# Performance work log

Hardware: AMD Instinct MI355X
Metric: run time of the kernel (lower is better)

The kernel has to match this reference:

```python
import jax, jax.numpy as jnp
import numpy as np

EPS = 1e-7
MIN_NORM = 1e-15
PROJ_EPS = 1e-5
NEG_SLOPE = 0.2
HEADS = 4


def artanh(x):
    return jnp.arctanh(jnp.clip(x, -1.0 + EPS, 1.0 - EPS))


def _norm(x):
    return jnp.clip(jnp.linalg.norm(x, axis=-1, keepdims=True), MIN_NORM)


def proj(x):
    # project onto Poincare ball (c=1)
    n = _norm(x)
    maxn = 1.0 - PROJ_EPS
    return jnp.where(n > maxn, x / n * maxn, x)


def expmap0(u):
    n = _norm(u)
    return jnp.tanh(n) * u / n


def logmap0(x):
    n = _norm(x)
    return artanh(n) * x / n


def mobius_add(x, y):
    x2 = jnp.sum(x * x, axis=-1, keepdims=True)
    y2 = jnp.sum(y * y, axis=-1, keepdims=True)
    xy = jnp.sum(x * y, axis=-1, keepdims=True)
    num = (1.0 + 2.0 * xy + y2) * x + (1.0 - x2) * y
    den = 1.0 + 2.0 * xy + x2 * y2
    return num / jnp.clip(den, MIN_NORM)


def pdist(x, y):
    # Poincare distance, c=1 -> [...,] scalar
    ma = mobius_add(-x, y)
    return 2.0 * artanh(jnp.linalg.norm(ma, axis=-1))


def mobius_scalar_mul(r, x):
    n = _norm(x)
    return jnp.tanh(r * artanh(n)) * x / n


def mobius_matvec(W, x):
    # x: [N,din], W: [dout,din]
    mx = x @ W.T
    n_x = _norm(x)
    n_mx = _norm(mx)
    return jnp.tanh(n_mx / n_x * artanh(n_x)) * mx / n_mx


def segment_softmax(logits, seg, num_segments):
    m = jax.ops.segment_max(logits, seg, num_segments=num_segments)
    m = jnp.where(jnp.isfinite(m), m, 0.0)
    e = jnp.exp(logits - m[seg])
    s = jax.ops.segment_sum(e, seg, num_segments=num_segments)
    return e / (s[seg] + 1e-16)


def setup_inputs() -> dict:
    N, E, D = 50000, 500000, 128
    H = HEADS
    Dh = D // H
    ks = jax.random.split(jax.random.key(0), 12)
    # edges without self-loops (reference re-adds them, mirroring remove/add_self_loops)
    src = jax.random.randint(ks[0], (E,), 0, N)
    off = jax.random.randint(ks[1], (E,), 1, N)
    dst = (src + off) % N
    edge_index = jnp.stack([src, dst]).astype(jnp.int32)
    x_e = 0.1 * jax.random.normal(ks[2], (N, D), dtype=jnp.float32)
    x_h = proj(expmap0(0.05 * jax.random.normal(ks[3], (N, D), dtype=jnp.float32)))
    sc = 1.0 / np.sqrt(D)
    W_e = sc * jax.random.normal(ks[4], (D, D), dtype=jnp.float32)
    b_lin_e = jnp.zeros((D,), jnp.float32)
    att_e = 0.1 * jax.random.normal(ks[5], (1, H, 2 * Dh), dtype=jnp.float32)
    b_e = jnp.zeros((D,), jnp.float32)
    W_h = sc * jax.random.normal(ks[6], (D, D), dtype=jnp.float32)
    b_lin_h = jnp.zeros((D,), jnp.float32)
    att_h = 0.1 * jax.random.normal(ks[7], (1, H, 2 * Dh), dtype=jnp.float32)
    b_h = jnp.zeros((D,), jnp.float32)
    att_hf = 0.1 * jax.random.normal(ks[8], (1, 1), dtype=jnp.float32)
    att_ef = 0.1 * jax.random.normal(ks[9], (1, 1), dtype=jnp.float32)
    return {"x_e": x_e, "x_h": x_h, "edge_index": edge_index,
            "W_e": W_e, "b_lin_e": b_lin_e, "att_e": att_e, "b_e": b_e,
            "W_h": W_h, "b_lin_h": b_lin_h, "att_h": att_h, "b_h": b_h,
            "att_hf": att_hf, "att_ef": att_ef}


def reference(x_e, x_h, edge_index, W_e, b_lin_e, att_e, b_e,
              W_h, b_lin_h, att_h, b_h, att_hf, att_ef):
    N, D = x_e.shape
    H = HEADS
    Dh = att_e.shape[-1] // 2
    loop = jnp.arange(N, dtype=edge_index.dtype)
    src = jnp.concatenate([edge_index[0], loop])  # j (source)
    dst = jnp.concatenate([edge_index[1], loop])  # i (target, softmax segment)

    # ---- Euclidean GAT branch (GATConv) ----
    xe = (x_e @ W_e.T + b_lin_e).reshape(N, H, Dh)
    a_i = jnp.sum(xe * att_e[:, :, :Dh], axis=-1)  # [N,H] target part
    a_j = jnp.sum(xe * att_e[:, :, Dh:], axis=-1)  # [N,H] source part
    alpha = jax.nn.leaky_relu(a_i[dst] + a_j[src], NEG_SLOPE)  # [E',H]
    alpha = segment_softmax(alpha, dst, N)
    agg = jax.ops.segment_sum(xe[src] * alpha[:, :, None], dst, num_segments=N)
    e_out = jax.nn.relu(agg.reshape(N, H * Dh) + b_e)

    # ---- Hyperbolic GAT branch (HGATConv with HypLinear) ----
    mv = proj(mobius_matvec(W_h, x_h))
    hb = proj(expmap0(b_lin_h))  # proj_tan0 is identity on Poincare ball
    xh = proj(mobius_add(mv, hb))  # [N,D] hyperbolic points (original_x)
    lx = logmap0(xh).reshape(N, H, Dh)
    hi = jnp.sum(lx * att_h[:, :, :Dh], axis=-1)
    hj = jnp.sum(lx * att_h[:, :, Dh:], axis=-1)
    alpha_h = hi[dst] + hj[src]  # [E',H]
    d = pdist(xh[dst], xh[src])  # [E'] hyperbolic edge distances
    d = segment_softmax(d, dst, N)[:, None]
    alpha_h = jax.nn.leaky_relu(alpha_h * d, NEG_SLOPE)
    alpha_h = segment_softmax(alpha_h, dst, N)
    agg_h = jax.ops.segment_sum(lx[src] * alpha_h[:, :, None], dst, num_segments=N)
    out_t = jax.nn.relu(agg_h.reshape(N, H * Dh) + b_h)  # tangent at origin
    h_out = proj(expmap0(out_t))

    # ---- HFusion: fuse Euclidean into hyperbolic ----
    ye = proj(expmap0(e_out))
    dist_f = (pdist(h_out, ye) * att_hf[0, 0])[:, None]  # [N,1]
    xe2 = proj(mobius_scalar_mul(dist_f, ye))
    h_fused = proj(mobius_add(h_out, xe2))

    # ---- EFusion: fuse hyperbolic into Euclidean ----
    lh = logmap0(h_out)
    de = (jnp.sum((lh - e_out) ** 2, axis=-1) * att_ef[0, 0])[:, None]
    e_fused = e_out + de * lh

    return jnp.stack([h_fused, e_fused])  # [2,N,D]
```

## Files before the change

### kernel.cpp

```cpp
#include <hip/hip_runtime.h>
#include <hip/hip_fp16.h>
#include <math.h>

typedef _Float16 h2 __attribute__((ext_vector_type(2)));
typedef _Float16 h8 __attribute__((ext_vector_type(8)));
typedef float f32x4 __attribute__((ext_vector_type(4)));

#define MAXN_BALL (1.0f - 1e-5f)
#define ART_CLIP  (1.0f - 1e-7f)
#define MAXD 48

__device__ __forceinline__ float f_rcp(float x)  { return __builtin_amdgcn_rcpf(x); }
__device__ __forceinline__ float f_exp(float x)  { return __expf(x); }
__device__ __forceinline__ float f_log(float x)  { return __logf(x); }
__device__ __forceinline__ float f_tanh(float x) {
    float ax = fabsf(x);
    float e = __expf(2.f * ax);
    float t = 1.f - 2.f * f_rcp(e + 1.f);
    return copysignf(t, x);
}
__device__ __forceinline__ float f_atanh(float x) {
    x = fminf(x, ART_CLIP);
    return 0.5f * f_log((1.f + x) * f_rcp(1.f - x));
}
__device__ __forceinline__ float leaky(float x) { return x > 0.0f ? x : 0.2f * x; }

union F4H8 { float4 f; h2 h[4]; };
union F2H4 { float2 f; h2 h[2]; };
union H8U  { h8 v; h2 h[4]; };

__device__ __forceinline__ h2 pk16(float x, float y) {
    union { decltype(__builtin_amdgcn_cvt_pkrtz(0.f, 0.f)) a; h2 b; } u;
    u.a = __builtin_amdgcn_cvt_pkrtz(x, y);
    return u.b;
}

__global__ __launch_bounds__(256) void k_prep(const float* __restrict__ X0,
                                              const float* __restrict__ X1,
                                              const float* __restrict__ W0,
                                              const float* __restrict__ W1,
                                              const float* __restrict__ bias0,
                                              h2* __restrict__ Y0,
                                              h2* __restrict__ Y1,
                                              int* __restrict__ counts,
                                              int N) {
    int t = threadIdx.x;
    if (blockIdx.y == 0) {
        int zi = blockIdx.x * 256 + t;
        if (zi < N) counts[zi] = 0;
    }
    int wv = t >> 6, l = t & 63;
    int rt = blockIdx.x * 4 + wv;
    if (rt * 16 >= N) return;
    int mat = blockIdx.y;
    const float* X = mat ? X1 : X0;
    const float* W = mat ? W1 : W0;
    h2* Y = mat ? Y1 : Y0;

    int lane16 = l & 15, quad = l >> 4;
    int r = rt * 16 + lane16;
    int rr = (r < N) ? r : (N - 1);
    const float* Xrow = &X[(size_t)rr * 128 + quad * 8];

    H8U bfr[4];
#pragma unroll
    for (int ks = 0; ks < 4; ++ks) {
        float4 xa = *(const float4*)(Xrow + ks * 32);
        float4 xb = *(const float4*)(Xrow + ks * 32 + 4);
        bfr[ks].h[0] = pk16(xa.x, xa.y); bfr[ks].h[1] = pk16(xa.z, xa.w);
        bfr[ks].h[2] = pk16(xb.x, xb.y); bfr[ks].h[3] = pk16(xb.z, xb.w);
    }

#pragma unroll
    for (int ct = 0; ct < 8; ++ct) {
        int o = ct * 16 + lane16;
        const float* Wrow = &W[(size_t)o * 128 + quad * 8];
        f32x4 acc = {0.f, 0.f, 0.f, 0.f};
#pragma unroll
        for (int ks = 0; ks < 4; ++ks) {
            float4 wa = *(const float4*)(Wrow + ks * 32);
            float4 wb = *(const float4*)(Wrow + ks * 32 + 4);
            H8U a;
            a.h[0] = pk16(wa.x, wa.y); a.h[1] = pk16(wa.z, wa.w);
            a.h[2] = pk16(wb.x, wb.y); a.h[3] = pk16(wb.z, wb.w);
            acc = __builtin_amdgcn_mfma_f32_16x16x32_f16(a.v, bfr[ks].v, acc, 0, 0, 0);
        }
        int obase = ct * 16 + quad * 4;
        float b0 = 0.f, b1 = 0.f, b2 = 0.f, b3 = 0.f;
        if (mat == 0) {
            b0 = bias0[obase]; b1 = bias0[obase + 1];
            b2 = bias0[obase + 2]; b3 = bias0[obase + 3];
        }
        if (r < N) {
            F2H4 u;
            u.h[0] = pk16(acc[0] + b0, acc[1] + b1);
            u.h[1] = pk16(acc[2] + b2, acc[3] + b3);
            *(float2*)&Y[(size_t)r * 64 + (obase >> 1)] = u.f;
        }
    }
}

__global__ __launch_bounds__(256) void k_node1_scatter(
        const h2* __restrict__ xe16, const float* __restrict__ x_h,
        const h2* __restrict__ mx16, h2* __restrict__ xh16,
        float* __restrict__ aux_j, float* __restrict__ aux_i,
        const float* __restrict__ att_e, const float* __restrict__ att_h,
        const float* __restrict__ b_lin_h,
        const int* __restrict__ ei, int* __restrict__ counts,
        int* __restrict__ srcs,
        int N, int E, int nblocks) {
    int t = threadIdx.x;
    int bx = blockIdx.x;
    if (bx >= nblocks) {
        int idx = (bx - nblocks) * 256 + t;
        if (idx < E + N) {
            int s, d;
            if (idx < E) { s = ei[idx]; d = ei[E + idx]; } else { s = d = idx - E; }
            int p = atomicAdd(&counts[d], 1);
            if (p < MAXD) srcs[d * MAXD + p] = s;
        }
        return;
    }
    int sl = t & 31, ni = t >> 5;
    int i = bx * 8 + ni;
    if (i >= N) return;
    int ht = sl >> 3, d0 = (sl & 7) * 4;

    F2H4 uxe; uxe.f = *(const float2*)&xe16[(size_t)i * 64 + 2 * sl];
    float4 xe4 = make_float4((float)uxe.h[0].x, (float)uxe.h[0].y,
                             (float)uxe.h[1].x, (float)uxe.h[1].y);
    float4 aeT = *(const float4*)&att_e[ht * 64 + d0];
    float4 aeS = *(const float4*)&att_e[ht * 64 + 32 + d0];
    float pi = xe4.x * aeT.x + xe4.y * aeT.y + xe4.z * aeT.z + xe4.w * aeT.w;
    float pj = xe4.x * aeS.x + xe4.y * aeS.y + xe4.z * aeS.z + xe4.w * aeS.w;
#pragma unroll
    for (int m = 1; m <= 4; m <<= 1) { pi += __shfl_xor(pi, m, 64); pj += __shfl_xor(pj, m, 64); }

    F2H4 umx; umx.f = *(const float2*)&mx16[(size_t)i * 64 + 2 * sl];
    float4 mx4 = make_float4((float)umx.h[0].x, (float)umx.h[0].y,
                             (float)umx.h[1].x, (float)umx.h[1].y);
    float4 xv4 = *(const float4*)&x_h[(size_t)i * 128 + 4 * sl];
    float4 bv4 = *(const float4*)&b_lin_h[4 * sl];
    float nx2  = xv4.x * xv4.x + xv4.y * xv4.y + xv4.z * xv4.z + xv4.w * xv4.w;
    float nmx2 = mx4.x * mx4.x + mx4.y * mx4.y + mx4.z * mx4.z + mx4.w * mx4.w;
    float nb2  = bv4.x * bv4.x + bv4.y * bv4.y + bv4.z * bv4.z + bv4.w * bv4.w;
    float dmb  = mx4.x * bv4.x + mx4.y * bv4.y + mx4.z * bv4.z + mx4.w * bv4.w;
#pragma unroll
    for (int m = 16; m >= 1; m >>= 1) {
        nx2 += __shfl_xor(nx2, m, 64); nmx2 += __shfl_xor(nmx2, m, 64);
        nb2 += __shfl_xor(nb2, m, 64); dmb  += __shfl_xor(dmb, m, 64);
    }

    float nxr = sqrtf(nx2),  nxc = fmaxf(nxr, 1e-15f);
    float nmxr = sqrtf(nmx2), nmxc = fmaxf(nmxr, 1e-15f);
    float tt = f_tanh(nmxc * f_rcp(nxc) * f_atanh(nxc));
    float c_m = tt * f_rcp(nmxc);
    float nmv = tt * (nmxr * f_rcp(nmxc));
    if (nmv > MAXN_BALL) { c_m *= MAXN_BALL / nmv; nmv = MAXN_BALL; }

    float nbr = sqrtf(nb2), nbc = fmaxf(nbr, 1e-15f);
    float tb = f_tanh(nbc);
    float c_b = tb * f_rcp(nbc);
    float nhb = tb * (nbr * f_rcp(nbc));
    if (nhb > MAXN_BALL) { c_b *= MAXN_BALL / nhb; nhb = MAXN_BALL; }

    float xy = c_m * c_b * dmb;
    float x2 = nmv * nmv, y2 = nhb * nhb;
    float den = fmaxf(1.f + 2.f * xy + x2 * y2, 1e-15f);
    float rden = f_rcp(den);
    float al = (1.f + 2.f * xy + y2) * c_m * rden;
    float be = (1.f - x2) * c_b * rden;
    float nr2 = al * al * nmx2 + 2.f * al * be * dmb + be * be * nb2;
    float nrr = sqrtf(nr2);
    if (nrr > MAXN_BALL) { float sc = MAXN_BALL / nrr; al *= sc; be *= sc; }
    float4 resv;
    resv.x = al * mx4.x + be * bv4.x; resv.y = al * mx4.y + be * bv4.y;
    resv.z = al * mx4.z + be * bv4.z; resv.w = al * mx4.w + be * bv4.w;
    F2H4 st;
    st.h[0] = pk16(resv.x, resv.y);
    st.h[1] = pk16(resv.z, resv.w);
    *(float2*)&xh16[(size_t)i * 64 + 2 * sl] = st.f;
    float4 rv = make_float4((float)st.h[0].x, (float)st.h[0].y,
                            (float)st.h[1].x, (float)st.h[1].y);

    float nr2r = rv.x * rv.x + rv.y * rv.y + rv.z * rv.z + rv.w * rv.w;
#pragma unroll
    for (int m = 16; m >= 1; m >>= 1) nr2r += __shfl_xor(nr2r, m, 64);
    float nrrr = sqrtf(nr2r);
    float nnc = fmaxf(nrrr, 1e-15f);
    float lam = f_atanh(nnc) * f_rcp(nnc);
    if (sl == 0) { aux_j[(size_t)i * 16 + 8] = lam; aux_j[(size_t)i * 16 + 9] = nr2r; }

    float4 lxv = make_float4(lam * rv.x, lam * rv.y, lam * rv.z, lam * rv.w);
    float4 ahT = *(const float4*)&att_h[ht * 64 + d0];
    float4 ahS = *(const float4*)&att_h[ht * 64 + 32 + d0];
    float qi = lxv.x * ahT.x + lxv.y * ahT.y + lxv.z * ahT.z + lxv.w * ahT.w;
    float qj = lxv.x * ahS.x + lxv.y * ahS.y + lxv.z * ahS.z + lxv.w * ahS.w;
#pragma unroll
    for (int m = 1; m <= 4; m <<= 1) { qi += __shfl_xor(qi, m, 64); qj += __shfl_xor(qj, m, 64); }
    if ((sl & 7) == 0) {
        aux_j[(size_t)i * 16 + ht] = qj;
        aux_j[(size_t)i * 16 + 4 + ht] = pj;
        aux_i[(size_t)i * 8 + ht] = qi;
        aux_i[(size_t)i * 8 + 4 + ht] = pi;
    }
}

__global__ __launch_bounds__(256) void k_node_final(
    const h2* __restrict__ xh16, const float* __restrict__ aux_j,
    const float* __restrict__ aux_i, const h2* __restrict__ xe16,
    const int* __restrict__ counts, const int* __restrict__ srcs,
    const float* __restrict__ b_e, const float* __restrict__ b_h,
    const float* __restrict__ att_hf, const float* __restrict__ att_ef,
    float* __restrict__ out, int N) {
    __shared__ int   s_src_all[8][MAXD];
    __shared__ float s_d_all[8][MAXD];
    __shared__ float s_ah_all[8][MAXD * 4];
    __shared__ float s_ae_all[8][MAXD * 4];

    int t = threadIdx.x;
    int sl = t & 31, ni = t >> 5;
    int i = blockIdx.x * 8 + ni;
    if (i >= N) return;
    int*   s_src = s_src_all[ni];
    float* s_d   = s_d_all[ni];
    float* s_ah  = s_ah_all[ni];
    float* s_ae  = s_ae_all[ni];

    int deg = counts[i];
    if (deg > MAXD) deg = MAXD;
    if (sl < deg)      s_src[sl]      = srcs[i * MAXD + sl];
    if (sl + 32 < deg) s_src[sl + 32] = srcs[i * MAXD + sl + 32];

    float x2i = aux_j[(size_t)i * 16 + 9];
    {
        int g = sl & 7, sub = sl >> 3;
        const h2* xi = &xh16[(size_t)i * 64 + g * 8];
        F4H8 us0, us1;
        us0.f = *(const float4*)xi;
        us1.f = *(const float4*)(xi + 4);
        for (int p = 0; p * 4 < deg; ++p) {
            int e = p * 4 + sub;
            bool act = e < deg;
            float dot = 0.f;
            int j = 0;
            if (act) {
                j = s_src[e];
                const h2* rp = &xh16[(size_t)j * 64 + g * 8];
                F4H8 ua, ub;
                ua.f = *(const float4*)rp;
                ub.f = *(const float4*)(rp + 4);
#pragma unroll
                for (int k = 0; k < 4; ++k) dot = __builtin_amdgcn_fdot2(ua.h[k], us0.h[k], dot, false);
#pragma unroll
                for (int k = 0; k < 4; ++k) dot = __builtin_amdgcn_fdot2(ub.h[k], us1.h[k], dot, false);
            }
            dot += __shfl_xor(dot, 1, 64);
            dot += __shfl_xor(dot, 2, 64);
            dot += __shfl_xor(dot, 4, 64);
            if (act && g == 0) {
                float y2 = aux_j[(size_t)j * 16 + 9];
                float xy = dot;
                float A = 1.f - 2.f * xy + y2;
                float B = 1.f - x2i;
                float den = fmaxf(1.f - 2.f * xy + x2i * y2, 1e-15f);
                float num2 = fmaxf(A * A * x2i - 2.f * A * B * xy + B * B * y2, 0.f);
                float nma = fminf(sqrtf(num2) * f_rcp(den), ART_CLIP);
                s_d[e] = f_log((1.f + nma) * f_rcp(1.f - nma));
            }
        }
    }

    float eA = (sl < deg)      ? f_exp(s_d[sl])      : 0.f;
    float eB = (sl + 32 < deg) ? f_exp(s_d[sl + 32]) : 0.f;
    float ssum = eA + eB;
#pragma unroll
    for (int m = 16; m >= 1; m >>= 1) ssum += __shfl_xor(ssum, m, 64);
    float dinv = f_rcp(ssum + 1e-16f);

    float4 hi4 = *(const float4*)&aux_i[(size_t)i * 8];
    float4 ai4 = *(const float4*)&aux_i[(size_t)i * 8 + 4];
    float4 vh_s[2], ve_s[2];
    float lam_s[2] = {0.f, 0.f};
    float4 sh = make_float4(0.f, 0.f, 0.f, 0.f), se = sh;
#pragma unroll
    for (int s = 0; s < 2; ++s) {
        int e = sl + 32 * s;
        if (e < deg) {
            int j = s_src[e];
            float ds = (s ? eB : eA) * dinv;
            float4 hj4 = *(const float4*)&aux_j[(size_t)j * 16];
            float4 aj4 = *(const float4*)&aux_j[(size_t)j * 16 + 4];
            lam_s[s] = aux_j[(size_t)j * 16 + 8];
            float4 vh, ve;
            vh.x = f_exp(leaky((hi4.x + hj4.x) * ds));
            vh.y = f_exp(leaky((hi4.y + hj4.y) * ds));
            vh.z = f_exp(leaky((hi4.z + hj4.z) * ds));
            vh.w = f_exp(leaky((hi4.w + hj4.w) * ds));
            ve.x = f_exp(leaky(ai4.x + aj4.x));
            ve.y = f_exp(leaky(ai4.y + aj4.y));
            ve.z = f_exp(leaky(ai4.z + aj4.z));
            ve.w = f_exp(leaky(ai4.w + aj4.w));
            vh_s[s] = vh; ve_s[s] = ve;
            sh.x += vh.x; sh.y += vh.y; sh.z += vh.z; sh.w += vh.w;
            se.x += ve.x; se.y += ve.y; se.z += ve.z; se.w += ve.w;
        }
    }
#pragma unroll
    for (int m = 16; m >= 1; m >>= 1) {
        sh.x += __shfl_xor(sh.x, m, 64); sh.y += __shfl_xor(sh.y, m, 64);
        sh.z += __shfl_xor(sh.z, m, 64); sh.w += __shfl_xor(sh.w, m, 64);
        se.x += __shfl_xor(se.x, m, 64); se.y += __shfl_xor(se.y, m, 64);
        se.z += __shfl_xor(se.z, m, 64); se.w += __shfl_xor(se.w, m, 64);
    }
    float4 rh = make_float4(f_rcp(sh.x + 1e-16f), f_rcp(sh.y + 1e-16f),
                            f_rcp(sh.z + 1e-16f), f_rcp(sh.w + 1e-16f));
    float4 re = make_float4(f_rcp(se.x + 1e-16f), f_rcp(se.y + 1e-16f),
                            f_rcp(se.z + 1e-16f), f_rcp(se.w + 1e-16f));
#pragma unroll
    for (int s = 0; s < 2; ++s) {
        int e = sl + 32 * s;
        if (e < deg) {
            float lamj = lam_s[s];
            float4 vh = vh_s[s], ve = ve_s[s];
            vh.x *= rh.x * lamj; vh.y *= rh.y * lamj; vh.z *= rh.z * lamj; vh.w *= rh.w * lamj;
            ve.x *= re.x; ve.y *= re.y; ve.z *= re.z; ve.w *= re.w;
            *(float4*)&s_ah[e * 4] = vh;
            *(float4*)&s_ae[e * 4] = ve;
        }
    }

    int hq = sl >> 3;
    float4 aE = make_float4(0.f, 0.f, 0.f, 0.f), aH = aE;
    int e = 0;
    for (; e + 1 < deg; e += 2) {
        int j0 = s_src[e], j1 = s_src[e + 1];
        F2H4 ux0, uh0, ux1, uh1;
        ux0.f = *(const float2*)&xe16[(size_t)j0 * 64 + 2 * sl];
        uh0.f = *(const float2*)&xh16[(size_t)j0 * 64 + 2 * sl];
        ux1.f = *(const float2*)&xe16[(size_t)j1 * 64 + 2 * sl];
        uh1.f = *(const float2*)&xh16[(size_t)j1 * 64 + 2 * sl];
        float we0 = s_ae[e * 4 + hq], wh0 = s_ah[e * 4 + hq];
        float we1 = s_ae[(e + 1) * 4 + hq], wh1 = s_ah[(e + 1) * 4 + hq];
        aE.x += we0 * (float)ux0.h[0].x + we1 * (float)ux1.h[0].x;
        aE.y += we0 * (float)ux0.h[0].y + we1 * (float)ux1.h[0].y;
        aE.z += we0 * (float)ux0.h[1].x + we1 * (float)ux1.h[1].x;
        aE.w += we0 * (float)ux0.h[1].y + we1 * (float)ux1.h[1].y;
        aH.x += wh0 * (float)uh0.h[0].x + wh1 * (float)uh1.h[0].x;
        aH.y += wh0 * (float)uh0.h[0].y + wh1 * (float)uh1.h[0].y;
        aH.z += wh0 * (float)uh0.h[1].x + wh1 * (float)uh1.h[1].x;
        aH.w += wh0 * (float)uh0.h[1].y + wh1 * (float)uh1.h[1].y;
    }
    if (e < deg) {
        int j = s_src[e];
        F2H4 ux, uh;
        ux.f = *(const float2*)&xe16[(size_t)j * 64 + 2 * sl];
        uh.f = *(const float2*)&xh16[(size_t)j * 64 + 2 * sl];
        float we = s_ae[e * 4 + hq], wh = s_ah[e * 4 + hq];
        aE.x += we * (float)ux.h[0].x; aE.y += we * (float)ux.h[0].y;
        aE.z += we * (float)ux.h[1].x; aE.w += we * (float)ux.h[1].y;
        aH.x += wh * (float)uh.h[0].x; aH.y += wh * (float)uh.h[0].y;
        aH.z += wh * (float)uh.h[1].x; aH.w += wh * (float)uh.h[1].y;
    }

    float4 be4 = *(const float4*)&b_e[4 * sl];
    float4 bh4 = *(const float4*)&b_h[4 * sl];
    float4 eo, ot;
    eo.x = fmaxf(aE.x + be4.x, 0.f); eo.y = fmaxf(aE.y + be4.y, 0.f);
    eo.z = fmaxf(aE.z + be4.z, 0.f); eo.w = fmaxf(aE.w + be4.w, 0.f);
    ot.x = fmaxf(aH.x + bh4.x, 0.f); ot.y = fmaxf(aH.y + bh4.y, 0.f);
    ot.z = fmaxf(aH.z + bh4.z, 0.f); ot.w = fmaxf(aH.w + bh4.w, 0.f);
    float n2  = ot.x * ot.x + ot.y * ot.y + ot.z * ot.z + ot.w * ot.w;
    float ne2 = eo.x * eo.x + eo.y * eo.y + eo.z * eo.z + eo.w * eo.w;
    float dot3 = ot.x * eo.x + ot.y * eo.y + ot.z * eo.z + ot.w * eo.w;
#pragma unroll
    for (int m = 16; m >= 1; m >>= 1) {
        n2 += __shfl_xor(n2, m, 64); ne2 += __shfl_xor(ne2, m, 64); dot3 += __shfl_xor(dot3, m, 64);
    }

    float n_raw = sqrtf(n2), n_c = fmaxf(n_raw, 1e-15f);
    float th = f_tanh(n_c);
    float c_h = th * f_rcp(n_c);
    float nh = th * (n_raw * f_rcp(n_c));
    if (nh > MAXN_BALL) { c_h *= MAXN_BALL / nh; nh = MAXN_BALL; }

    float nE_raw = sqrtf(ne2), nE_c = fmaxf(nE_raw, 1e-15f);
    float tE = f_tanh(nE_c);
    float c_e = tE * f_rcp(nE_c);
    float ny = tE * (nE_raw * f_rcp(nE_c));
    if (ny > MAXN_BALL) { c_e *= MAXN_BALL / ny; ny = MAXN_BALL; }

    float xyv = c_h * c_e * dot3;
    float x2f = nh * nh, y2f = ny * ny;
    float A = 1.f - 2.f * xyv + y2f, B = 1.f - x2f;
    float den = fmaxf(1.f - 2.f * xyv + x2f * y2f, 1e-15f);
    float num2 = fmaxf(A * A * x2f - 2.f * A * B * xyv + B * B * y2f, 0.f);
    float nma = fminf(sqrtf(num2) * f_rcp(den), ART_CLIP);
    float distf = f_log((1.f + nma) * f_rcp(1.f - nma)) * att_hf[0];
    float nyc = fmaxf(ny, 1e-15f);
    float s1 = f_tanh(distf * f_atanh(nyc)) * f_rcp(nyc);
    float nxe2 = fabsf(s1) * ny;
    if (nxe2 > MAXN_BALL) { s1 *= MAXN_BALL / nxe2; nxe2 = MAXN_BALL; }
    float xy2 = s1 * xyv;
    float y22 = nxe2 * nxe2;
    float rden2 = f_rcp(fmaxf(1.f + 2.f * xy2 + x2f * y22, 1e-15f));
    float alpha = (1.f + 2.f * xy2 + y22) * rden2 * c_h;
    float beta  = (1.f - x2f) * s1 * rden2 * c_e;
    float nf2 = alpha * alpha * n2 + 2.f * alpha * beta * dot3 + beta * beta * ne2;
    float nf = sqrtf(nf2);
    if (nf > MAXN_BALL) { float sc = MAXN_BALL / nf; alpha *= sc; beta *= sc; }

    float nhc = fmaxf(nh, 1e-15f);
    float gam = f_atanh(nhc) * f_rcp(nhc) * c_h;
    float de2 = gam * gam * n2 - 2.f * gam * dot3 + ne2;
    float dg = de2 * att_ef[0] * gam;

    float4 o1;
    o1.x = alpha * ot.x + beta * eo.x; o1.y = alpha * ot.y + beta * eo.y;
    o1.z = alpha * ot.z + beta * eo.z; o1.w = alpha * ot.w + beta * eo.w;
    *(float4*)&out[(size_t)i * 128 + 4 * sl] = o1;
    float4 o2;
    o2.x = eo.x + dg * ot.x; o2.y = eo.y + dg * ot.y;
    o2.z = eo.z + dg * ot.z; o2.w = eo.w + dg * ot.w;
    *(float4*)&out[(size_t)N * 128 + (size_t)i * 128 + 4 * sl] = o2;
}

extern "C" void kernel_launch(void* const* d_in, const int* in_sizes, int n_in,
                              void* d_out, int out_size, void* d_ws, size_t ws_size,
                              hipStream_t stream) {
    const float* x_e      = (const float*)d_in[0];
    const float* x_h      = (const float*)d_in[1];
    const int*   ei       = (const int*)d_in[2];
    const float* W_e      = (const float*)d_in[3];
    const float* b_lin_e  = (const float*)d_in[4];
    const float* att_e    = (const float*)d_in[5];
    const float* b_e      = (const float*)d_in[6];
    const float* W_h      = (const float*)d_in[7];
    const float* b_lin_h  = (const float*)d_in[8];
    const float* att_h    = (const float*)d_in[9];
    const float* b_h      = (const float*)d_in[10];
    const float* att_hf   = (const float*)d_in[11];
    const float* att_ef   = (const float*)d_in[12];

    int N = in_sizes[0] / 128;
    int E = in_sizes[2] / 2;
    int EN = E + N;

    char* ws = (char*)d_ws;
    size_t off = 0;
    auto alloc = [&](size_t bytes) -> void* {
        void* p = ws + off;
        off = (off + bytes + 255) & ~(size_t)255;
        return p;
    };
    h2*    xe16  = (h2*)alloc((size_t)N * 128 * 2);
    h2*    mx16  = (h2*)alloc((size_t)N * 128 * 2);
    h2*    xh16  = (h2*)alloc((size_t)N * 128 * 2);
    float* aux_j = (float*)alloc((size_t)N * 16 * 4);
    float* aux_i = (float*)alloc((size_t)N * 8 * 4);
    int*   counts= (int*)alloc((size_t)N * 4);
    int*   srcs  = (int*)alloc((size_t)N * MAXD * 4);

    int rtiles = (N + 15) / 16;
    int rblocks = (rtiles + 3) / 4;
    dim3 pgrid(rblocks, 2);
    k_prep<<<pgrid, 256, 0, stream>>>(x_e, x_h, W_e, W_h, b_lin_e,
                                      xe16, mx16, counts, N);

    int nblocks = (N + 7) / 8;
    int eblocks = (EN + 255) / 256;
    k_node1_scatter<<<nblocks + eblocks, 256, 0, stream>>>(
        xe16, x_h, mx16, xh16, aux_j, aux_i,
        att_e, att_h, b_lin_h, ei, counts, srcs, N, E, nblocks);

    int fblocks = (N + 7) / 8;
    k_node_final<<<fblocks, 256, 0, stream>>>(xh16, aux_j, aux_i, xe16,
                                              counts, srcs, b_e, b_h, att_hf, att_ef,
                                              (float*)d_out, N);
}
```

Baseline: 290.4 us.

## Interleave Euclidean and hyperbolic fp16 features into one buffer; unroll distance loop

```diff
diff --git a/kernel.cpp b/kernel.cpp
--- a/kernel.cpp
+++ b/kernel.cpp
@@ -40,8 +40,7 @@
                                               const float* __restrict__ W0,
                                               const float* __restrict__ W1,
                                               const float* __restrict__ bias0,
-                                              h2* __restrict__ Y0,
-                                              h2* __restrict__ Y1,
+                                              float* __restrict__ xd,
                                               int* __restrict__ counts,
                                               int N) {
     int t = threadIdx.x;
@@ -55,7 +54,6 @@
     int mat = blockIdx.y;
     const float* X = mat ? X1 : X0;
     const float* W = mat ? W1 : W0;
-    h2* Y = mat ? Y1 : Y0;
 
     int lane16 = l & 15, quad = l >> 4;
     int r = rt * 16 + lane16;
@@ -95,14 +93,14 @@
             F2H4 u;
             u.h[0] = pk16(acc[0] + b0, acc[1] + b1);
             u.h[1] = pk16(acc[2] + b2, acc[3] + b3);
-            *(float2*)&Y[(size_t)r * 64 + (obase >> 1)] = u.f;
+            *(float2*)&xd[(size_t)r * 128 + obase + (mat ? 2 : 0)] = u.f;
         }
     }
 }
 
 __global__ __launch_bounds__(256) void k_node1_scatter(
-        const h2* __restrict__ xe16, const float* __restrict__ x_h,
-        const h2* __restrict__ mx16, h2* __restrict__ xh16,
+        float* __restrict__ xd, const float* __restrict__ x_h,
+        h2* __restrict__ xh16,
         float* __restrict__ aux_j, float* __restrict__ aux_i,
         const float* __restrict__ att_e, const float* __restrict__ att_h,
         const float* __restrict__ b_lin_h,
@@ -126,7 +124,7 @@
     if (i >= N) return;
     int ht = sl >> 3, d0 = (sl & 7) * 4;
 
-    F2H4 uxe; uxe.f = *(const float2*)&xe16[(size_t)i * 64 + 2 * sl];
+    F2H4 uxe; uxe.f = *(const float2*)&xd[(size_t)i * 128 + 4 * sl];
     float4 xe4 = make_float4((float)uxe.h[0].x, (float)uxe.h[0].y,
                              (float)uxe.h[1].x, (float)uxe.h[1].y);
     float4 aeT = *(const float4*)&att_e[ht * 64 + d0];
@@ -136,7 +134,7 @@
 #pragma unroll
     for (int m = 1; m <= 4; m <<= 1) { pi += __shfl_xor(pi, m, 64); pj += __shfl_xor(pj, m, 64); }
 
-    F2H4 umx; umx.f = *(const float2*)&mx16[(size_t)i * 64 + 2 * sl];
+    F2H4 umx; umx.f = *(const float2*)&xd[(size_t)i * 128 + 4 * sl + 2];
     float4 mx4 = make_float4((float)umx.h[0].x, (float)umx.h[0].y,
                              (float)umx.h[1].x, (float)umx.h[1].y);
     float4 xv4 = *(const float4*)&x_h[(size_t)i * 128 + 4 * sl];
@@ -180,6 +178,7 @@
     st.h[0] = pk16(resv.x, resv.y);
     st.h[1] = pk16(resv.z, resv.w);
     *(float2*)&xh16[(size_t)i * 64 + 2 * sl] = st.f;
+    *(float2*)&xd[(size_t)i * 128 + 4 * sl + 2] = st.f;
     float4 rv = make_float4((float)st.h[0].x, (float)st.h[0].y,
                             (float)st.h[1].x, (float)st.h[1].y);
 
@@ -207,8 +206,8 @@
 }
 
 __global__ __launch_bounds__(256) void k_node_final(
-    const h2* __restrict__ xh16, const float* __restrict__ aux_j,
-    const float* __restrict__ aux_i, const h2* __restrict__ xe16,
+    const h2* __restrict__ xh16, const float* __restrict__ xd,
+    const float* __restrict__ aux_j, const float* __restrict__ aux_i,
     const int* __restrict__ counts, const int* __restrict__ srcs,
     const float* __restrict__ b_e, const float* __restrict__ b_h,
     const float* __restrict__ att_hf, const float* __restrict__ att_ef,
@@ -239,34 +238,61 @@
         F4H8 us0, us1;
         us0.f = *(const float4*)xi;
         us1.f = *(const float4*)(xi + 4);
-        for (int p = 0; p * 4 < deg; ++p) {
-            int e = p * 4 + sub;
-            bool act = e < deg;
-            float dot = 0.f;
-            int j = 0;
-            if (act) {
-                j = s_src[e];
-                const h2* rp = &xh16[(size_t)j * 64 + g * 8];
-                F4H8 ua, ub;
-                ua.f = *(const float4*)rp;
-                ub.f = *(const float4*)(rp + 4);
-#pragma unroll
-                for (int k = 0; k < 4; ++k) dot = __builtin_amdgcn_fdot2(ua.h[k], us0.h[k], dot, false);
-#pragma unroll
-                for (int k = 0; k < 4; ++k) dot = __builtin_amdgcn_fdot2(ub.h[k], us1.h[k], dot, false);
+        for (int p = 0; p * 8 < deg; ++p) {
+            int e0 = p * 8 + sub;
+            int e1 = e0 + 4;
+            bool a0 = e0 < deg, a1 = e1 < deg;
+            float dot0 = 0.f, dot1 = 0.f;
+            int j0 = 0, j1 = 0;
+            F4H8 ua0, ub0, ua1, ub1;
+            if (a0) {
+                j0 = s_src[e0];
+                const h2* rp = &xh16[(size_t)j0 * 64 + g * 8];
+                ua0.f = *(const float4*)rp;
+                ub0.f = *(const float4*)(rp + 4);
             }
-            dot += __shfl_xor(dot, 1, 64);
-            dot += __shfl_xor(dot, 2, 64);
-            dot += __shfl_xor(dot, 4, 64);
-            if (act && g == 0) {
-                float y2 = aux_j[(size_t)j * 16 + 9];
-                float xy = dot;
-                float A = 1.f - 2.f * xy + y2;
-                float B = 1.f - x2i;
-                float den = fmaxf(1.f - 2.f * xy + x2i * y2, 1e-15f);
-                float num2 = fmaxf(A * A * x2i - 2.f * A * B * xy + B * B * y2, 0.f);
-                float nma = fminf(sqrtf(num2) * f_rcp(den), ART_CLIP);
-                s_d[e] = f_log((1.f + nma) * f_rcp(1.f - nma));
+            if (a1) {
+                j1 = s_src[e1];
+                const h2* rp = &xh16[(size_t)j1 * 64 + g * 8];
+                ua1.f = *(const float4*)rp;
+                ub1.f = *(const float4*)(rp + 4);
+            }
+            if (a0) {
+#pragma unroll
+                for (int k = 0; k < 4; ++k) dot0 = __builtin_amdgcn_fdot2(ua0.h[k], us0.h[k], dot0, false);
+#pragma unroll
+                for (int k = 0; k < 4; ++k) dot0 = __builtin_amdgcn_fdot2(ub0.h[k], us1.h[k], dot0, false);
+            }
+            if (a1) {
+#pragma unroll
+                for (int k = 0; k < 4; ++k) dot1 = __builtin_amdgcn_fdot2(ua1.h[k], us0.h[k], dot1, false);
+#pragma unroll
+                for (int k = 0; k < 4; ++k) dot1 = __builtin_amdgcn_fdot2(ub1.h[k], us1.h[k], dot1, false);
+            }
+            dot0 += __shfl_xor(dot0, 1, 64); dot1 += __shfl_xor(dot1, 1, 64);
+            dot0 += __shfl_xor(dot0, 2, 64); dot1 += __shfl_xor(dot1, 2, 64);
+            dot0 += __shfl_xor(dot0, 4, 64); dot1 += __shfl_xor(dot1, 4, 64);
+            if (g == 0) {
+                if (a0) {
+                    float y2 = aux_j[(size_t)j0 * 16 + 9];
+                    float xy = dot0;
+                    float A = 1.f - 2.f * xy + y2;
+                    float B = 1.f - x2i;
+                    float den = fmaxf(1.f - 2.f * xy + x2i * y2, 1e-15f);
+                    float num2 = fmaxf(A * A * x2i - 2.f * A * B * xy + B * B * y2, 0.f);
+                    float nma = fminf(sqrtf(num2) * f_rcp(den), ART_CLIP);
+                    s_d[e0] = f_log((1.f + nma) * f_rcp(1.f - nma));
+                }
+                if (a1) {
+                    float y2 = aux_j[(size_t)j1 * 16 + 9];
+                    float xy = dot1;
+                    float A = 1.f - 2.f * xy + y2;
+                    float B = 1.f - x2i;
+                    float den = fmaxf(1.f - 2.f * xy + x2i * y2, 1e-15f);
+                    float num2 = fmaxf(A * A * x2i - 2.f * A * B * xy + B * B * y2, 0.f);
+                    float nma = fminf(sqrtf(num2) * f_rcp(den), ART_CLIP);
+                    s_d[e1] = f_log((1.f + nma) * f_rcp(1.f - nma));
+                }
             }
         }
     }
@@ -335,32 +361,29 @@
     int e = 0;
     for (; e + 1 < deg; e += 2) {
         int j0 = s_src[e], j1 = s_src[e + 1];
-        F2H4 ux0, uh0, ux1, uh1;
-        ux0.f = *(const float2*)&xe16[(size_t)j0 * 64 + 2 * sl];
-        uh0.f = *(const float2*)&xh16[(size_t)j0 * 64 + 2 * sl];
-        ux1.f = *(const float2*)&xe16[(size_t)j1 * 64 + 2 * sl];
-        uh1.f = *(const float2*)&xh16[(size_t)j1 * 64 + 2 * sl];
+        F4H8 u0, u1;
+        u0.f = *(const float4*)&xd[(size_t)j0 * 128 + 4 * sl];
+        u1.f = *(const float4*)&xd[(size_t)j1 * 128 + 4 * sl];
         float we0 = s_ae[e * 4 + hq], wh0 = s_ah[e * 4 + hq];
         float we1 = s_ae[(e + 1) * 4 + hq], wh1 = s_ah[(e + 1) * 4 + hq];
-        aE.x += we0 * (float)ux0.h[0].x + we1 * (float)ux1.h[0].x;
-        aE.y += we0 * (float)ux0.h[0].y + we1 * (float)ux1.h[0].y;
-        aE.z += we0 * (float)ux0.h[1].x + we1 * (float)ux1.h[1].x;
-        aE.w += we0 * (float)ux0.h[1].y + we1 * (float)ux1.h[1].y;
-        aH.x += wh0 * (float)uh0.h[0].x + wh1 * (float)uh1.h[0].x;
-        aH.y += wh0 * (float)uh0.h[0].y + wh1 * (float)uh1.h[0].y;
-        aH.z += wh0 * (float)uh0.h[1].x + wh1 * (float)uh1.h[1].x;
-        aH.w += wh0 * (float)uh0.h[1].y + wh1 * (float)uh1.h[1].y;
+        aE.x += we0 * (float)u0.h[0].x + we1 * (float)u1.h[0].x;
+        aE.y += we0 * (float)u0.h[0].y + we1 * (float)u1.h[0].y;
+        aE.z += we0 * (float)u0.h[1].x + we1 * (float)u1.h[1].x;
+        aE.w += we0 * (float)u0.h[1].y + we1 * (float)u1.h[1].y;
+        aH.x += wh0 * (float)u0.h[2].x + wh1 * (float)u1.h[2].x;
+        aH.y += wh0 * (float)u0.h[2].y + wh1 * (float)u1.h[2].y;
+        aH.z += wh0 * (float)u0.h[3].x + wh1 * (float)u1.h[3].x;
+        aH.w += wh0 * (float)u0.h[3].y + wh1 * (float)u1.h[3].y;
     }
     if (e < deg) {
         int j = s_src[e];
-        F2H4 ux, uh;
-        ux.f = *(const float2*)&xe16[(size_t)j * 64 + 2 * sl];
-        uh.f = *(const float2*)&xh16[(size_t)j * 64 + 2 * sl];
+        F4H8 u0;
+        u0.f = *(const float4*)&xd[(size_t)j * 128 + 4 * sl];
         float we = s_ae[e * 4 + hq], wh = s_ah[e * 4 + hq];
-        aE.x += we * (float)ux.h[0].x; aE.y += we * (float)ux.h[0].y;
-        aE.z += we * (float)ux.h[1].x; aE.w += we * (float)ux.h[1].y;
-        aH.x += wh * (float)uh.h[0].x; aH.y += wh * (float)uh.h[0].y;
-        aH.z += wh * (float)uh.h[1].x; aH.w += wh * (float)uh.h[1].y;
+        aE.x += we * (float)u0.h[0].x; aE.y += we * (float)u0.h[0].y;
+        aE.z += we * (float)u0.h[1].x; aE.w += we * (float)u0.h[1].y;
+        aH.x += wh * (float)u0.h[2].x; aH.y += wh * (float)u0.h[2].y;
+        aH.z += wh * (float)u0.h[3].x; aH.w += wh * (float)u0.h[3].y;
     }
 
     float4 be4 = *(const float4*)&b_e[4 * sl];
@@ -453,9 +476,8 @@
         off = (off + bytes + 255) & ~(size_t)255;
         return p;
     };
-    h2*    xe16  = (h2*)alloc((size_t)N * 128 * 2);
-    h2*    mx16  = (h2*)alloc((size_t)N * 128 * 2);
     h2*    xh16  = (h2*)alloc((size_t)N * 128 * 2);
+    float* xd    = (float*)alloc((size_t)N * 128 * 4);
     float* aux_j = (float*)alloc((size_t)N * 16 * 4);
     float* aux_i = (float*)alloc((size_t)N * 8 * 4);
     int*   counts= (int*)alloc((size_t)N * 4);
@@ -465,16 +487,16 @@
     int rblocks = (rtiles + 3) / 4;
     dim3 pgrid(rblocks, 2);
     k_prep<<<pgrid, 256, 0, stream>>>(x_e, x_h, W_e, W_h, b_lin_e,
-                                      xe16, mx16, counts, N);
+                                      xd, counts, N);
 
     int nblocks = (N + 7) / 8;
     int eblocks = (EN + 255) / 256;
     k_node1_scatter<<<nblocks + eblocks, 256, 0, stream>>>(
-        xe16, x_h, mx16, xh16, aux_j, aux_i,
+        xd, x_h, xh16, aux_j, aux_i,
         att_e, att_h, b_lin_h, ei, counts, srcs, N, E, nblocks);
 
     int fblocks = (N + 7) / 8;
-    k_node_final<<<fblocks, 256, 0, stream>>>(xh16, aux_j, aux_i, xe16,
+    k_node_final<<<fblocks, 256, 0, stream>>>(xh16, xd, aux_j, aux_i,
                                               counts, srcs, b_e, b_h, att_hf, att_ef,
                                               (float*)d_out, N);
 }
```

Result: slower. 303.9 us (+4.6%).
